# Kernel tuning notes

Measured on AMD Instinct MI355X. Metric: run time of the kernel, lower is better.

The kernel has to match this reference:

```python
import jax, jax.numpy as jnp
import numpy as np

BATCH = 4096
IN_DIM = 512
OUT_DIM = 512
GRID_SIZE = 5
K = 3


def _extended_grid():
    # Original: grid = linspace(-1, 1, grid_size+1), spacing h = 2/grid_size.
    # The de Boor-Cox recursion in the source indexes up to grid[grid_size+2k],
    # so we extend the uniform grid to the right with the same spacing.
    h = 2.0 / GRID_SIZE
    return (-1.0 + h * jnp.arange(GRID_SIZE + 2 * K + 1)).astype(jnp.float32)


def bspline_basis(x, grid, k):
    """Vectorized de Boor-Cox recursion.
    x: [..., ] floats; returns basis [..., grid_size + k].
    Identical math to the recursive b_spline_basis in the source, but computed
    bottom-up over all knot intervals at once (no redundant recomputation).
    """
    xe = x[..., None]  # [..., 1]
    # degree-0: indicator of half-open knot intervals, [..., n_knots-1]
    B = ((grid[:-1] <= xe) & (xe < grid[1:])).astype(x.dtype)
    for d in range(1, k + 1):
        n = grid.shape[0] - d - 1
        gi, gid = grid[:n], grid[d:d + n]          # grid[i], grid[i+d]
        gi1, gid1 = grid[1:n + 1], grid[d + 1:d + n + 1]  # grid[i+1], grid[i+d+1]
        # uniform grid -> denominators are d*h, never zero
        B = (xe - gi) / (gid - gi) * B[..., :n] + (gid1 - xe) / (gid1 - gi1) * B[..., 1:n + 1]
    return B  # [..., grid_size + k]


def setup_inputs() -> dict:
    key = jax.random.key(0)
    k1, k2 = jax.random.split(key)
    x = jax.random.uniform(k1, (BATCH, IN_DIM), jnp.float32) * 2.0 - 1.0  # in [-1, 1)
    spline_coeff = jax.random.normal(k2, (IN_DIM, OUT_DIM, GRID_SIZE + K), jnp.float32)
    spline_scaling = jnp.ones((IN_DIM, OUT_DIM), jnp.float32)
    return {"x": x, "spline_coeff": spline_coeff, "spline_scaling": spline_scaling}


def reference(x, spline_coeff, spline_scaling):
    grid = _extended_grid()
    basis = bspline_basis(x, grid, K)  # [B, in_dim, grid_size+k]
    # out[b, j] = sum_i scaling[i,j] * sum_g basis[b,i,g] * coeff[i,j,g]
    return jnp.einsum('big,ijg,ij->bj', basis, spline_coeff, spline_scaling)
```

## Files before the change

### kernel.cpp

```cpp
#include <hip/hip_runtime.h>
#include <hip/hip_bf16.h>
#include <stdint.h>


#define BATCH   4096
#define IN_DIM  512
#define OUT_DIM 512
#define KDIM    (IN_DIM * 8)
#define NKT     (KDIM / 64)

typedef short short8 __attribute__((ext_vector_type(8)));
typedef float f32x4  __attribute__((ext_vector_type(4)));

#define WAIT_VM8 0xF78
#define WAIT_VM4 0xF74
#define WAIT_VM0 0xF70

__device__ __forceinline__ unsigned short f2bf(float f) {
  union { float f; unsigned int u; } v; v.f = f;
  unsigned int r = v.u + 0x7FFFu + ((v.u >> 16) & 1u);
  return (unsigned short)(r >> 16);
}

__device__ __forceinline__ void bspline_win(float xv, float* w, int* mm) {
  float t = (xv + 1.0f) * 2.5f;
  int m = (int)t;
  m = m < 0 ? 0 : (m > 4 ? 4 : m);
  float u  = t - (float)m;
  float u2 = u * u, u3 = u2 * u, om = 1.0f - u;
  w[0] = om * om * om * (1.0f / 6.0f);
  w[1] = (3.0f * u3 - 6.0f * u2 + 4.0f) * (1.0f / 6.0f);
  w[2] = (-3.0f * u3 + 3.0f * u2 + 3.0f * u + 1.0f) * (1.0f / 6.0f);
  w[3] = u3 * (1.0f / 6.0f);
  *mm = m;
}

__device__ __forceinline__ short8 basis_pack8(float xv) {
  float w[4]; int m;
  bspline_win(xv, w, &m);
  short8 h = {};
#pragma unroll
  for (int g = 0; g < 8; ++g) {
    int d = g - m + 3;
    float v = (d == 0) ? w[0] : (d == 1) ? w[1] : (d == 2) ? w[2] : (d == 3) ? w[3] : 0.0f;
    h[g] = (short)f2bf(v);
  }
  return h;
}

__device__ __forceinline__ void async_load16(const void* g, void* l) {
  __builtin_amdgcn_global_load_lds(
      (__attribute__((address_space(1))) void*)(uintptr_t)g,
      (__attribute__((address_space(3))) void*)(unsigned int)(uintptr_t)l,
      16, 0, 0);
}

__global__ void kan_prep(const float* __restrict__ x,
                         const float* __restrict__ coeff,
                         const float* __restrict__ scaling,
                         unsigned short* __restrict__ Ag,
                         unsigned short* __restrict__ Wt) {
  const int b = blockIdx.x;
  if (b < (BATCH * IN_DIM) / 256) {
    int idx = b * 256 + threadIdx.x;
    short8 h = basis_pack8(x[idx]);
    *reinterpret_cast<short8*>(Ag + (size_t)idx * 8) = h;
  } else {
    int idx = (b - (BATCH * IN_DIM) / 256) * 256 + threadIdx.x;
    int i = idx >> 9, j = idx & 511;
    float s = scaling[idx];
    const float4* cp = reinterpret_cast<const float4*>(coeff) + (size_t)idx * 2;
    float4 c0 = cp[0], c1 = cp[1];
    short8 h;
    h[0] = (short)f2bf(c0.x * s); h[1] = (short)f2bf(c0.y * s);
    h[2] = (short)f2bf(c0.z * s); h[3] = (short)f2bf(c0.w * s);
    h[4] = (short)f2bf(c1.x * s); h[5] = (short)f2bf(c1.y * s);
    h[6] = (short)f2bf(c1.z * s); h[7] = (short)f2bf(c1.w * s);
    *reinterpret_cast<short8*>(Wt + (size_t)j * KDIM + i * 8) = h;
  }
}

__global__ __launch_bounds__(256, 2)
void kan_gemm_p(const unsigned short* __restrict__ Ag,
                const unsigned short* __restrict__ Wt,
                float* __restrict__ out) {
  __shared__ unsigned short As[3][64 * 64];
  __shared__ unsigned short Bs[3][64 * 64];

  const int tid  = threadIdx.x;
  const int lane = tid & 63;
  const int wid  = tid >> 6;
  const int wm = wid >> 1, wn = wid & 1;
  const int ln = lane & 15, quad = lane >> 4;

  const int b    = blockIdx.x;
  const int row0 = (b & 63) * 64;
  const int col0 = (b >> 6) * 64;

  f32x4 acc[2][2] = {};

  const int lr = lane >> 3;
  const int cg = (lane & 7) ^ lr;

  const unsigned short* aRow = Ag + (size_t)(row0 + wid * 16 + lr) * KDIM + cg * 8;
  const unsigned short* bRow = Wt + (size_t)(col0 + wid * 16 + lr) * KDIM + cg * 8;

  auto issue = [&](int kt, int st) {
    const int k0 = kt * 64;
#pragma unroll
    for (int t = 0; t < 2; ++t) {
      const int rbase = wid * 16 + t * 8;
      async_load16(aRow + (size_t)t * 8 * KDIM + k0, &As[st][rbase * 64]);
      async_load16(bRow + (size_t)t * 8 * KDIM + k0, &Bs[st][rbase * 64]);
    }
  };

  auto compute = [&](int st) {
#pragma unroll
    for (int kk = 0; kk < 2; ++kk) {
      short8 af[2], bfr[2];
#pragma unroll
      for (int mt = 0; mt < 2; ++mt) {
        const int r    = wm * 32 + mt * 16 + ln;
        const int slot = (kk * 4 + quad) ^ (r & 7);
        af[mt] = *reinterpret_cast<const short8*>(&As[st][r * 64 + slot * 8]);
      }
#pragma unroll
      for (int nt = 0; nt < 2; ++nt) {
        const int c    = wn * 32 + nt * 16 + ln;
        const int slot = (kk * 4 + quad) ^ (c & 7);
        bfr[nt] = *reinterpret_cast<const short8*>(&Bs[st][c * 64 + slot * 8]);
      }
#pragma unroll
      for (int mt = 0; mt < 2; ++mt)
#pragma unroll
        for (int nt = 0; nt < 2; ++nt)
          acc[mt][nt] = __builtin_amdgcn_mfma_f32_16x16x32_bf16(af[mt], bfr[nt], acc[mt][nt], 0, 0, 0);
    }
  };

  issue(0, 0); issue(1, 1); issue(2, 2);

  int st = 0;
  for (int kt = 0; kt < NKT - 3; ++kt) {
    __builtin_amdgcn_s_waitcnt(WAIT_VM8);
    __builtin_amdgcn_s_barrier();
    compute(st);
    __builtin_amdgcn_s_barrier();
    issue(kt + 3, st);
    st = (st == 2) ? 0 : st + 1;
  }
  __builtin_amdgcn_s_waitcnt(WAIT_VM8);
  __builtin_amdgcn_s_barrier();
  compute(st);
  st = (st == 2) ? 0 : st + 1;
  __builtin_amdgcn_s_waitcnt(WAIT_VM4);
  __builtin_amdgcn_s_barrier();
  compute(st);
  st = (st == 2) ? 0 : st + 1;
  __builtin_amdgcn_s_waitcnt(WAIT_VM0);
  __builtin_amdgcn_s_barrier();
  compute(st);

#pragma unroll
  for (int mt = 0; mt < 2; ++mt)
#pragma unroll
    for (int nt = 0; nt < 2; ++nt) {
      const int col = col0 + wn * 32 + nt * 16 + ln;
#pragma unroll
      for (int r = 0; r < 4; ++r) {
        const int row = row0 + wm * 32 + mt * 16 + quad * 4 + r;
        out[(size_t)row * OUT_DIM + col] = acc[mt][nt][r];
      }
    }
}

__global__ __launch_bounds__(256, 2)
void kan_gemm_fb(const float* __restrict__ x, const float* __restrict__ coeff,
                 const float* __restrict__ scaling, float* __restrict__ out) {
  __shared__ unsigned short As[64 * 64];
  __shared__ unsigned short Bs[64 * 64];

  const int tid  = threadIdx.x;
  const int lane = tid & 63;
  const int wid  = tid >> 6;
  const int wm = wid >> 1, wn = wid & 1;
  const int ln = lane & 15, quad = lane >> 4;
  const int row0 = blockIdx.y * 64;
  const int col0 = blockIdx.x * 64;

  f32x4 acc[2][2] = {};

  for (int kt = 0; kt < KDIM / 64; ++kt) {
#pragma unroll
    for (int pp = 0; pp < 2; ++pp) {
      const int p  = tid + pp * 256;
      const int rn = p & 63;
      const int il = p >> 6;
      const int sw = ((il ^ (rn & 7)) * 8);
      short8 ha = basis_pack8(x[(size_t)(row0 + rn) * IN_DIM + kt * 8 + il]);
      *reinterpret_cast<short8*>(&As[rn * 64 + sw]) = ha;
      const float* cbase = coeff + (size_t)(kt * 8 + il) * 4096 + (size_t)(col0 + rn) * 8;
      float4 c0 = reinterpret_cast<const float4*>(cbase)[0];
      float4 c1 = reinterpret_cast<const float4*>(cbase)[1];
      float s = scaling[(size_t)(kt * 8 + il) * OUT_DIM + col0 + rn];
      short8 hb;
      hb[0] = (short)f2bf(c0.x * s); hb[1] = (short)f2bf(c0.y * s);
      hb[2] = (short)f2bf(c0.z * s); hb[3] = (short)f2bf(c0.w * s);
      hb[4] = (short)f2bf(c1.x * s); hb[5] = (short)f2bf(c1.y * s);
      hb[6] = (short)f2bf(c1.z * s); hb[7] = (short)f2bf(c1.w * s);
      *reinterpret_cast<short8*>(&Bs[rn * 64 + sw]) = hb;
    }
    __syncthreads();
#pragma unroll
    for (int kk = 0; kk < 2; ++kk) {
      short8 af[2], bfr[2];
#pragma unroll
      for (int mt = 0; mt < 2; ++mt) {
        const int r  = wm * 32 + mt * 16 + ln;
        const int pc = (kk * 4 + quad) ^ (r & 7);
        af[mt] = *reinterpret_cast<const short8*>(&As[r * 64 + pc * 8]);
      }
#pragma unroll
      for (int nt = 0; nt < 2; ++nt) {
        const int c  = wn * 32 + nt * 16 + ln;
        const int pc = (kk * 4 + quad) ^ (c & 7);
        bfr[nt] = *reinterpret_cast<const short8*>(&Bs[c * 64 + pc * 8]);
      }
#pragma unroll
      for (int mt = 0; mt < 2; ++mt)
#pragma unroll
        for (int nt = 0; nt < 2; ++nt)
          acc[mt][nt] = __builtin_amdgcn_mfma_f32_16x16x32_bf16(af[mt], bfr[nt], acc[mt][nt], 0, 0, 0);
    }
    __syncthreads();
  }
#pragma unroll
  for (int mt = 0; mt < 2; ++mt)
#pragma unroll
    for (int nt = 0; nt < 2; ++nt) {
      const int col = col0 + wn * 32 + nt * 16 + ln;
#pragma unroll
      for (int r = 0; r < 4; ++r) {
        const int row = row0 + wm * 32 + mt * 16 + quad * 4 + r;
        out[(size_t)row * OUT_DIM + col] = acc[mt][nt][r];
      }
    }
}

extern "C" void kernel_launch(void* const* d_in, const int* in_sizes, int n_in,
                              void* d_out, int out_size, void* d_ws, size_t ws_size,
                              hipStream_t stream) {
  const float* x       = (const float*)d_in[0];
  const float* coeff   = (const float*)d_in[1];
  const float* scaling = (const float*)d_in[2];
  float* out = (float*)d_out;

  const size_t needA = (size_t)BATCH * KDIM * 2;
  const size_t needW = (size_t)OUT_DIM * KDIM * 2;

  if (ws_size >= needA + needW) {
    unsigned short* Ag = (unsigned short*)d_ws;
    unsigned short* Wt = (unsigned short*)((char*)d_ws + needA);
    kan_prep<<<(BATCH * IN_DIM) / 256 + (IN_DIM * OUT_DIM) / 256, 256, 0, stream>>>(
        x, coeff, scaling, Ag, Wt);
    kan_gemm_p<<<(BATCH / 64) * (OUT_DIM / 64), 256, 0, stream>>>(Ag, Wt, out);
  } else {
    kan_gemm_fb<<<dim3(OUT_DIM / 64, BATCH / 64), 256, 0, stream>>>(x, coeff, scaling, out);
  }
}
```

Baseline: 98.75 us.

## Fuse B-spline basis generation into GEMM tile loader, drop materialized A buffer

Instead of precomputing the bf16 basis matrix (BATCH x IN_DIM*8) into workspace and streaming it back through async LDS loads, the GEMM kernel now reads raw x values, evaluates the cubic B-spline weights in registers and writes the swizzled bf16 tile directly into LDS. Only the weight matrix still goes through the async pipeline, and the waitcnt schedule is reworked to account for the extra x loads. Basis packing is rewritten as a 64-bit shift of four packed bf16 weights rather than a per-element select. The goal is to remove the large write and reread of the basis buffer. In exchange, each output tile recomputes the basis for its rows (8x redundancy across column blocks) and ALU work is added inside the main loop.

```diff
diff --git a/kernel.cpp b/kernel.cpp
--- a/kernel.cpp
+++ b/kernel.cpp
@@ -12,40 +12,37 @@
 typedef short short8 __attribute__((ext_vector_type(8)));
 typedef float f32x4  __attribute__((ext_vector_type(4)));
 
-#define WAIT_VM8 0xF78
-#define WAIT_VM4 0xF74
-#define WAIT_VM0 0xF70
-
-__device__ __forceinline__ unsigned short f2bf(float f) {
+#define W_VM4_LG0 0x074
+#define W_VM5_LG0 0x075
+#define W_VM6_LG0 0x076
+#define W_VM7_LG0 0x077
+#define W_VM1_LG0 0x071
+
+__device__ __forceinline__ unsigned int f2bf(float f) {
   union { float f; unsigned int u; } v; v.f = f;
   unsigned int r = v.u + 0x7FFFu + ((v.u >> 16) & 1u);
-  return (unsigned short)(r >> 16);
-}
-
-__device__ __forceinline__ void bspline_win(float xv, float* w, int* mm) {
-  float t = (xv + 1.0f) * 2.5f;
+  return r >> 16;
+}
+
+__device__ __forceinline__ short8 basis_pack8(float xv) {
+  float t = __builtin_fmaf(xv, 2.5f, 2.5f);
   int m = (int)t;
   m = m < 0 ? 0 : (m > 4 ? 4 : m);
   float u  = t - (float)m;
   float u2 = u * u, u3 = u2 * u, om = 1.0f - u;
-  w[0] = om * om * om * (1.0f / 6.0f);
-  w[1] = (3.0f * u3 - 6.0f * u2 + 4.0f) * (1.0f / 6.0f);
-  w[2] = (-3.0f * u3 + 3.0f * u2 + 3.0f * u + 1.0f) * (1.0f / 6.0f);
-  w[3] = u3 * (1.0f / 6.0f);
-  *mm = m;
-}
-
-__device__ __forceinline__ short8 basis_pack8(float xv) {
-  float w[4]; int m;
-  bspline_win(xv, w, &m);
-  short8 h = {};
-#pragma unroll
-  for (int g = 0; g < 8; ++g) {
-    int d = g - m + 3;
-    float v = (d == 0) ? w[0] : (d == 1) ? w[1] : (d == 2) ? w[2] : (d == 3) ? w[3] : 0.0f;
-    h[g] = (short)f2bf(v);
-  }
-  return h;
+  float w0 = om * om * om * (1.0f / 6.0f);
+  float w1 = (3.0f * u3 - 6.0f * u2 + 4.0f) * (1.0f / 6.0f);
+  float w2 = (-3.0f * u3 + 3.0f * u2 + 3.0f * u + 1.0f) * (1.0f / 6.0f);
+  float w3 = u3 * (1.0f / 6.0f);
+  uint64_t wp = (uint64_t)f2bf(w0) | ((uint64_t)f2bf(w1) << 16)
+              | ((uint64_t)f2bf(w2) << 32) | ((uint64_t)f2bf(w3) << 48);
+  int sh = (m - 3) * 16;
+  uint64_t lo, hi;
+  if (sh >= 0) { lo = wp << sh; hi = (sh > 0) ? (wp >> (64 - sh)) : 0ull; }
+  else         { lo = wp >> (-sh); hi = 0ull; }
+  union { uint64_t q[2]; short8 s; } r;
+  r.q[0] = lo; r.q[1] = hi;
+  return r.s;
 }
 
 __device__ __forceinline__ void async_load16(const void* g, void* l) {
@@ -55,33 +52,24 @@
       16, 0, 0);
 }
 
-__global__ void kan_prep(const float* __restrict__ x,
-                         const float* __restrict__ coeff,
+__global__ void kan_prep(const float* __restrict__ coeff,
                          const float* __restrict__ scaling,
-                         unsigned short* __restrict__ Ag,
                          unsigned short* __restrict__ Wt) {
-  const int b = blockIdx.x;
-  if (b < (BATCH * IN_DIM) / 256) {
-    int idx = b * 256 + threadIdx.x;
-    short8 h = basis_pack8(x[idx]);
-    *reinterpret_cast<short8*>(Ag + (size_t)idx * 8) = h;
-  } else {
-    int idx = (b - (BATCH * IN_DIM) / 256) * 256 + threadIdx.x;
-    int i = idx >> 9, j = idx & 511;
-    float s = scaling[idx];
-    const float4* cp = reinterpret_cast<const float4*>(coeff) + (size_t)idx * 2;
-    float4 c0 = cp[0], c1 = cp[1];
-    short8 h;
-    h[0] = (short)f2bf(c0.x * s); h[1] = (short)f2bf(c0.y * s);
-    h[2] = (short)f2bf(c0.z * s); h[3] = (short)f2bf(c0.w * s);
-    h[4] = (short)f2bf(c1.x * s); h[5] = (short)f2bf(c1.y * s);
-    h[6] = (short)f2bf(c1.z * s); h[7] = (short)f2bf(c1.w * s);
-    *reinterpret_cast<short8*>(Wt + (size_t)j * KDIM + i * 8) = h;
-  }
+  int idx = blockIdx.x * 256 + threadIdx.x;
+  int i = idx >> 9, j = idx & 511;
+  float s = scaling[idx];
+  const float4* cp = reinterpret_cast<const float4*>(coeff) + (size_t)idx * 2;
+  float4 c0 = cp[0], c1 = cp[1];
+  short8 h;
+  h[0] = (short)f2bf(c0.x * s); h[1] = (short)f2bf(c0.y * s);
+  h[2] = (short)f2bf(c0.z * s); h[3] = (short)f2bf(c0.w * s);
+  h[4] = (short)f2bf(c1.x * s); h[5] = (short)f2bf(c1.y * s);
+  h[6] = (short)f2bf(c1.z * s); h[7] = (short)f2bf(c1.w * s);
+  *reinterpret_cast<short8*>(Wt + (size_t)j * KDIM + i * 8) = h;
 }
 
 __global__ __launch_bounds__(256, 2)
-void kan_gemm_p(const unsigned short* __restrict__ Ag,
+void kan_gemm_p(const float* __restrict__ x,
                 const unsigned short* __restrict__ Wt,
                 float* __restrict__ out) {
   __shared__ unsigned short As[3][64 * 64];
@@ -102,17 +90,31 @@
   const int lr = lane >> 3;
   const int cg = (lane & 7) ^ lr;
 
-  const unsigned short* aRow = Ag + (size_t)(row0 + wid * 16 + lr) * KDIM + cg * 8;
   const unsigned short* bRow = Wt + (size_t)(col0 + wid * 16 + lr) * KDIM + cg * 8;
 
-  auto issue = [&](int kt, int st) {
+  const int rn = lane;
+  const float* xRow = x + (size_t)(row0 + rn) * IN_DIM + wid * 2;
+  const int sw0 = ((wid * 2)     ^ (rn & 7)) * 8;
+  const int sw1 = ((wid * 2 + 1) ^ (rn & 7)) * 8;
+
+  auto issueB = [&](int kt, int st) {
     const int k0 = kt * 64;
 #pragma unroll
     for (int t = 0; t < 2; ++t) {
       const int rbase = wid * 16 + t * 8;
-      async_load16(aRow + (size_t)t * 8 * KDIM + k0, &As[st][rbase * 64]);
       async_load16(bRow + (size_t)t * 8 * KDIM + k0, &Bs[st][rbase * 64]);
     }
+  };
+
+  auto computeA = [&](float2 xv, int st) {
+    short8 h0 = basis_pack8(xv.x);
+    short8 h1 = basis_pack8(xv.y);
+    *reinterpret_cast<short8*>(&As[st][rn * 64 + sw0]) = h0;
+    *reinterpret_cast<short8*>(&As[st][rn * 64 + sw1]) = h1;
+  };
+
+  auto loadx = [&](int kt) -> float2 {
+    return *reinterpret_cast<const float2*>(xRow + kt * 8);
   };
 
   auto compute = [&](int st) {
@@ -139,27 +141,40 @@
     }
   };
 
-  issue(0, 0); issue(1, 1); issue(2, 2);
+  float2 x0 = loadx(0), x1 = loadx(1), x2 = loadx(2), xcur = loadx(3);
+  issueB(0, 0); issueB(1, 1); issueB(2, 2);
+  computeA(x0, 0); computeA(x1, 1); computeA(x2, 2);
 
   int st = 0;
-  for (int kt = 0; kt < NKT - 3; ++kt) {
-    __builtin_amdgcn_s_waitcnt(WAIT_VM8);
+  __builtin_amdgcn_s_waitcnt(W_VM4_LG0); __builtin_amdgcn_s_barrier();
+  compute(0); __builtin_amdgcn_s_barrier();
+  issueB(3, 0); { float2 xn = loadx(4); computeA(xcur, 0); xcur = xn; }
+  __builtin_amdgcn_s_waitcnt(W_VM5_LG0); __builtin_amdgcn_s_barrier();
+  compute(1); __builtin_amdgcn_s_barrier();
+  issueB(4, 1); { float2 xn = loadx(5); computeA(xcur, 1); xcur = xn; }
+  __builtin_amdgcn_s_waitcnt(W_VM6_LG0); __builtin_amdgcn_s_barrier();
+  compute(2); __builtin_amdgcn_s_barrier();
+  issueB(5, 2); { float2 xn = loadx(6); computeA(xcur, 2); xcur = xn; }
+
+  st = 0;
+  for (int kt = 3; kt <= NKT - 4; ++kt) {
+    __builtin_amdgcn_s_waitcnt(W_VM7_LG0);
     __builtin_amdgcn_s_barrier();
     compute(st);
     __builtin_amdgcn_s_barrier();
-    issue(kt + 3, st);
+    issueB(kt + 3, st);
+    const int kx = (kt + 4 < NKT) ? (kt + 4) : (NKT - 1);
+    float2 xn = loadx(kx);
+    computeA(xcur, st);
+    xcur = xn;
     st = (st == 2) ? 0 : st + 1;
   }
-  __builtin_amdgcn_s_waitcnt(WAIT_VM8);
-  __builtin_amdgcn_s_barrier();
-  compute(st);
-  st = (st == 2) ? 0 : st + 1;
-  __builtin_amdgcn_s_waitcnt(WAIT_VM4);
-  __builtin_amdgcn_s_barrier();
-  compute(st);
-  st = (st == 2) ? 0 : st + 1;
-  __builtin_amdgcn_s_waitcnt(WAIT_VM0);
-  __builtin_amdgcn_s_barrier();
+
+  __builtin_amdgcn_s_waitcnt(W_VM7_LG0); __builtin_amdgcn_s_barrier();
+  compute(st); st = (st == 2) ? 0 : st + 1;
+  __builtin_amdgcn_s_waitcnt(W_VM4_LG0); __builtin_amdgcn_s_barrier();
+  compute(st); st = (st == 2) ? 0 : st + 1;
+  __builtin_amdgcn_s_waitcnt(W_VM1_LG0); __builtin_amdgcn_s_barrier();
   compute(st);
 
 #pragma unroll
@@ -256,15 +271,12 @@
   const float* scaling = (const float*)d_in[2];
   float* out = (float*)d_out;
 
-  const size_t needA = (size_t)BATCH * KDIM * 2;
   const size_t needW = (size_t)OUT_DIM * KDIM * 2;
 
-  if (ws_size >= needA + needW) {
-    unsigned short* Ag = (unsigned short*)d_ws;
-    unsigned short* Wt = (unsigned short*)((char*)d_ws + needA);
-    kan_prep<<<(BATCH * IN_DIM) / 256 + (IN_DIM * OUT_DIM) / 256, 256, 0, stream>>>(
-        x, coeff, scaling, Ag, Wt);
-    kan_gemm_p<<<(BATCH / 64) * (OUT_DIM / 64), 256, 0, stream>>>(Ag, Wt, out);
+  if (ws_size >= needW) {
+    unsigned short* Wt = (unsigned short*)d_ws;
+    kan_prep<<<(IN_DIM * OUT_DIM) / 256, 256, 0, stream>>>(coeff, scaling, Wt);
+    kan_gemm_p<<<(BATCH / 64) * (OUT_DIM / 64), 256, 0, stream>>>(x, Wt, out);
   } else {
     kan_gemm_fb<<<dim3(OUT_DIM / 64, BATCH / 64), 256, 0, stream>>>(x, coeff, scaling, out);
   }
```

After: 127.6 us. +29.2%, slower.
